# Optimization experiments

Hardware: AMD Instinct MI355X
Metric: run time of the kernel (lower is better)

The kernel has to match this reference:

```python
import jax, jax.numpy as jnp
import numpy as np

S, W = 256, 64          # sentences per doc, words per sentence
V, E = 100000, 256      # vocab, embedding dim
HW, HS, C = 256, 256, 10  # word hidden, sentence hidden, num categories


def _gru_dir(x, Wih, Whh, bih, bhh, reverse):
    """Single-direction GRU, PyTorch gate order (r, z, n). x: [B, T, D] -> [B, T, H]."""
    B, T, D = x.shape
    H = Whh.shape[1]
    xg = jnp.einsum('btd,gd->tbg', x, Wih) + bih  # [T, B, 3H], precompute input gates

    def step(h, xt):
        hg = h @ Whh.T + bhh
        xr, xz, xn = jnp.split(xt, 3, axis=-1)
        hr, hz, hn = jnp.split(hg, 3, axis=-1)
        r = jax.nn.sigmoid(xr + hr)
        z = jax.nn.sigmoid(xz + hz)
        n = jnp.tanh(xn + r * hn)
        h_new = (1.0 - z) * n + z * h
        return h_new, h_new

    h0 = jnp.zeros((B, H), x.dtype)
    _, ys = jax.lax.scan(step, h0, xg, reverse=reverse)  # ys: [T, B, H] in time order
    return jnp.swapaxes(ys, 0, 1)


def _bi_gru(x, WihF, WhhF, bihF, bhhF, WihB, WhhB, bihB, bhhB):
    out_f = _gru_dir(x, WihF, WhhF, bihF, bhhF, reverse=False)
    out_b = _gru_dir(x, WihB, WhhB, bihB, bhhB, reverse=True)
    return jnp.concatenate([out_f, out_b], axis=-1)  # [B, T, 2H]


def _attn_pool(out, w, b):
    # Sequential(Linear(2H,1), Tanh) then softmax over seq dim, weighted sum
    scores = jnp.tanh(out @ w + b)           # [B, T, 1]
    a = jax.nn.softmax(scores, axis=1)       # softmax over time
    return jnp.sum(a * out, axis=1)          # [B, 2H]


def setup_inputs() -> dict:
    key = jax.random.key(0)
    ks = jax.random.split(key, 32)
    sc = 0.05
    d = {
        'tokens': jax.random.randint(ks[0], (S, W), 0, V),
        'emb': jax.random.normal(ks[1], (V, E), jnp.float32) * sc,
        'wWihF': jax.random.normal(ks[2], (3 * HW, E), jnp.float32) * sc,
        'wWhhF': jax.random.normal(ks[3], (3 * HW, HW), jnp.float32) * sc,
        'wBihF': jax.random.normal(ks[4], (3 * HW,), jnp.float32) * sc,
        'wBhhF': jax.random.normal(ks[5], (3 * HW,), jnp.float32) * sc,
        'wWihB': jax.random.normal(ks[6], (3 * HW, E), jnp.float32) * sc,
        'wWhhB': jax.random.normal(ks[7], (3 * HW, HW), jnp.float32) * sc,
        'wBihB': jax.random.normal(ks[8], (3 * HW,), jnp.float32) * sc,
        'wBhhB': jax.random.normal(ks[9], (3 * HW,), jnp.float32) * sc,
        'sWihF': jax.random.normal(ks[10], (3 * HS, 2 * HW), jnp.float32) * sc,
        'sWhhF': jax.random.normal(ks[11], (3 * HS, HS), jnp.float32) * sc,
        'sBihF': jax.random.normal(ks[12], (3 * HS,), jnp.float32) * sc,
        'sBhhF': jax.random.normal(ks[13], (3 * HS,), jnp.float32) * sc,
        'sWihB': jax.random.normal(ks[14], (3 * HS, 2 * HW), jnp.float32) * sc,
        'sWhhB': jax.random.normal(ks[15], (3 * HS, HS), jnp.float32) * sc,
        'sBihB': jax.random.normal(ks[16], (3 * HS,), jnp.float32) * sc,
        'sBhhB': jax.random.normal(ks[17], (3 * HS,), jnp.float32) * sc,
        'wAttW': jax.random.normal(ks[18], (2 * HW, 1), jnp.float32) * sc,
        'wAttB': jax.random.normal(ks[19], (1,), jnp.float32) * sc,
        'sAttW': jax.random.normal(ks[20], (2 * HS, 1), jnp.float32) * sc,
        'sAttB': jax.random.normal(ks[21], (1,), jnp.float32) * sc,
        'clsW': jax.random.normal(ks[22], (C, 2 * HS), jnp.float32) * sc,
        'clsB': jax.random.normal(ks[23], (C,), jnp.float32) * sc,
    }
    return d


def reference(tokens, emb, wWihF, wWhhF, wBihF, wBhhF, wWihB, wWhhB, wBihB, wBhhB,
              sWihF, sWhhF, sBihF, sBhhF, sWihB, sWhhB, sBihB, sBhhB,
              wAttW, wAttB, sAttW, sAttB, clsW, clsB):
    # word level: all sentences batched together (packed form of the Python loop)
    x = emb[tokens]                                             # [S, W, E]
    word_out = _bi_gru(x, wWihF, wWhhF, wBihF, wBhhF, wWihB, wWhhB, wBihB, wBhhB)  # [S, W, 2HW]
    sent_vecs = _attn_pool(word_out, wAttW, wAttB)              # [S, 2HW]
    # sentence level: single document
    sent_in = sent_vecs[None]                                   # [1, S, 2HW]
    sent_out = _bi_gru(sent_in, sWihF, sWhhF, sBihF, sBhhF, sWihB, sWhhB, sBihB, sBhhB)  # [1, S, 2HS]
    doc_vec = _attn_pool(sent_out, sAttW, sAttB)                # [1, 2HS]
    logits = doc_vec @ clsW.T + clsB                            # [1, C]
    return jax.nn.softmax(logits, axis=1)
```

## Files before the change

### kernel.cpp

```cpp
#include <hip/hip_runtime.h>
#include <stdint.h>

typedef unsigned short ushort_t;
typedef uint32_t u32;
typedef __bf16 bf16;
typedef bf16 bf16x8 __attribute__((ext_vector_type(8)));
typedef float f32x4 __attribute__((ext_vector_type(4)));
typedef ushort_t ushort8 __attribute__((ext_vector_type(8)));

__device__ __forceinline__ float b2f(ushort_t u) {
    u32 x = ((u32)u) << 16;
    return __builtin_bit_cast(float, x);
}
__device__ __forceinline__ ushort_t f2b(float f) {
    bf16 h = (bf16)f;
    return __builtin_bit_cast(ushort_t, h);
}
__device__ __forceinline__ float sigmoidf_(float x) { return 1.0f / (1.0f + __expf(-x)); }
__device__ __forceinline__ float tanhf_(float x) { return 1.0f - 2.0f / (1.0f + __expf(2.0f * x)); }

__device__ __forceinline__ ushort8 cvt8(const float* __restrict__ p) {
    float4 v0 = *(const float4*)p;
    float4 v1 = *(const float4*)(p + 4);
    ushort8 r;
    r[0] = f2b(v0.x); r[1] = f2b(v0.y); r[2] = f2b(v0.z); r[3] = f2b(v0.w);
    r[4] = f2b(v1.x); r[5] = f2b(v1.y); r[6] = f2b(v1.z); r[7] = f2b(v1.w);
    return r;
}

#define TPAD 40

__global__ __launch_bounds__(256) void gemm_xg(
    const float* __restrict__ A, const int* __restrict__ tok,
    const float* __restrict__ WF, const float* __restrict__ WB,
    const float* __restrict__ bF, const float* __restrict__ bB,
    ushort_t* __restrict__ C, int K)
{
    __shared__ ushort_t aT[128 * TPAD];
    __shared__ ushort_t bT[128 * TPAD];
    const int tid = threadIdx.x;
    const int lane = tid & 63, wv = tid >> 6;
    const int bn0 = blockIdx.x * 128;
    const int rm0 = blockIdx.y * 128;
    const int wm = (wv & 1) * 64, wn = (wv >> 1) * 64;

    f32x4 acc[4][4];
    f32x4 zero = {0.f, 0.f, 0.f, 0.f};
#pragma unroll
    for (int i = 0; i < 4; i++)
#pragma unroll
        for (int j = 0; j < 4; j++) acc[i][j] = zero;

    const int sr = tid >> 1;
    const int sk = (tid & 1) * 16;
    long arow = tok ? (long)tok[rm0 + sr] : (long)(rm0 + sr);
    const float* aSrc = A + arow * K + sk;
    int ng = bn0 + sr;
    const float* bSrc = (ng < 768 ? WF + (long)ng * K : WB + (long)(ng - 768) * K) + sk;

    const int nkc = K / 32;
    const int fm = lane & 15, fq = (lane >> 4) * 8;
    for (int kc = 0; kc < nkc; ++kc) {
        ushort8 av0 = cvt8(aSrc + kc * 32);
        ushort8 av1 = cvt8(aSrc + kc * 32 + 8);
        ushort8 bv0 = cvt8(bSrc + kc * 32);
        ushort8 bv1 = cvt8(bSrc + kc * 32 + 8);
        __syncthreads();
        *(ushort8*)(aT + sr * TPAD + sk) = av0;
        *(ushort8*)(aT + sr * TPAD + sk + 8) = av1;
        *(ushort8*)(bT + sr * TPAD + sk) = bv0;
        *(ushort8*)(bT + sr * TPAD + sk + 8) = bv1;
        __syncthreads();
        bf16x8 af[4], bfg[4];
#pragma unroll
        for (int i = 0; i < 4; i++)
            af[i] = __builtin_bit_cast(bf16x8, *(const ushort8*)(aT + (wm + i * 16 + fm) * TPAD + fq));
#pragma unroll
        for (int j = 0; j < 4; j++)
            bfg[j] = __builtin_bit_cast(bf16x8, *(const ushort8*)(bT + (wn + j * 16 + fm) * TPAD + fq));
#pragma unroll
        for (int i = 0; i < 4; i++)
#pragma unroll
            for (int j = 0; j < 4; j++)
                acc[i][j] = __builtin_amdgcn_mfma_f32_16x16x32_bf16(af[i], bfg[j], acc[i][j], 0, 0, 0);
    }
    const int fr0 = (lane >> 4) * 4;
#pragma unroll
    for (int j = 0; j < 4; j++) {
        int col = bn0 + wn + j * 16 + fm;
        float bias = (col < 768) ? bF[col] : bB[col - 768];
#pragma unroll
        for (int i = 0; i < 4; i++) {
#pragma unroll
            for (int r = 0; r < 4; r++) {
                int row = rm0 + wm + i * 16 + fr0 + r;
                C[(long)row * 1536 + col] = f2b(acc[i][j][r] + bias);
            }
        }
    }
}

#define HBS 264

template<int NS>
__global__ __launch_bounds__(512, 2) void gru_level(
    const float* __restrict__ WhhF, const float* __restrict__ WhhB,
    const float* __restrict__ bhhF, const float* __restrict__ bhhB,
    const ushort_t* __restrict__ xg,
    ushort_t* __restrict__ out,
    int T)
{
    __shared__ ushort_t hbf[2][16 * HBS];

    const int tid = threadIdx.x, lane = tid & 63, wv = tid >> 6;
    const int dir = blockIdx.x & 1;
    const int grp = blockIdx.x >> 1;
    const float* Whh = dir ? WhhB : WhhF;
    const float* bhh = dir ? bhhB : bhhF;
    const int dirOff = dir * 768;

    const int fm = lane & 15, fq = (lane >> 4) * 8;
    const int mgrp = lane >> 4;
    const int d0 = 32 * wv + fm;

    bf16x8 wfrag[6][8];
#pragma unroll
    for (int g = 0; g < 3; ++g)
#pragma unroll
        for (int t = 0; t < 2; ++t) {
            const float* wrow = Whh + (long)(g * 256 + 32 * wv + 16 * t + fm) * 256 + fq;
#pragma unroll
            for (int kc = 0; kc < 8; ++kc)
                wfrag[g * 2 + t][kc] = __builtin_bit_cast(bf16x8, cvt8(wrow + kc * 32));
        }

    float bhhv[3][2];
#pragma unroll
    for (int g = 0; g < 3; ++g)
#pragma unroll
        for (int t = 0; t < 2; ++t)
            bhhv[g][t] = bhh[g * 256 + d0 + 16 * t];

    for (int i = tid; i < 16 * HBS; i += 512) { hbf[0][i] = 0; hbf[1][i] = 0; }

    const ushort_t* xgm[NS];
    ushort_t* outm[NS];
#pragma unroll
    for (int m = 0; m < NS; ++m) {
        int s = grp * NS + m;
        xgm[m] = xg + (long)s * T * 1536 + dirOff;
        outm[m] = out + (long)s * T * 512 + dir * 256;
    }

    float h[NS][2];
    ushort_t xv[NS][3][2];
    ushort_t ostage[NS][2];
#pragma unroll
    for (int m = 0; m < NS; ++m) { h[m][0] = 0.f; h[m][1] = 0.f; }

    if (mgrp == 0) {
        const int tt0 = dir ? (T - 1) : 0;
#pragma unroll
        for (int m = 0; m < NS; ++m)
#pragma unroll
            for (int g = 0; g < 3; ++g)
#pragma unroll
                for (int t = 0; t < 2; ++t)
                    xv[m][g][t] = xgm[m][(long)tt0 * 1536 + g * 256 + d0 + 16 * t];
    }
    __syncthreads();

    for (int st = 0; st < T; ++st) {
        const int cur = st & 1, nxt = cur ^ 1;
        if (st > 0 && mgrp == 0) {
            const int tp = dir ? (T - st) : (st - 1);
#pragma unroll
            for (int m = 0; m < NS; ++m) {
                outm[m][(long)tp * 512 + d0] = ostage[m][0];
                outm[m][(long)tp * 512 + d0 + 16] = ostage[m][1];
            }
        }
        f32x4 acc[6];
        f32x4 zero = {0.f, 0.f, 0.f, 0.f};
#pragma unroll
        for (int gi = 0; gi < 6; ++gi) acc[gi] = zero;
#pragma unroll
        for (int kc = 0; kc < 8; ++kc) {
            bf16x8 a = __builtin_bit_cast(bf16x8,
                *(const ushort8*)(&hbf[cur][fm * HBS + kc * 32 + fq]));
#pragma unroll
            for (int gi = 0; gi < 6; ++gi)
                acc[gi] = __builtin_amdgcn_mfma_f32_16x16x32_bf16(a, wfrag[gi][kc], acc[gi], 0, 0, 0);
        }
        if (mgrp == 0) {
#pragma unroll
            for (int m = 0; m < NS; ++m)
#pragma unroll
                for (int t = 0; t < 2; ++t) {
                    float xr = b2f(xv[m][0][t]);
                    float xz = b2f(xv[m][1][t]);
                    float xn = b2f(xv[m][2][t]);
                    float r = sigmoidf_(xr + acc[0 + t][m] + bhhv[0][t]);
                    float z = sigmoidf_(xz + acc[2 + t][m] + bhhv[1][t]);
                    float n = tanhf_(xn + r * (acc[4 + t][m] + bhhv[2][t]));
                    h[m][t] = (1.f - z) * n + z * h[m][t];
                    ushort_t hb = f2b(h[m][t]);
                    hbf[nxt][m * HBS + d0 + 16 * t] = hb;
                    ostage[m][t] = hb;
                }
            const int stn = (st + 1 < T) ? (st + 1) : st;
            const int ttn = dir ? (T - 1 - stn) : stn;
#pragma unroll
            for (int m = 0; m < NS; ++m)
#pragma unroll
                for (int g = 0; g < 3; ++g)
#pragma unroll
                    for (int t = 0; t < 2; ++t)
                        xv[m][g][t] = xgm[m][(long)ttn * 1536 + g * 256 + d0 + 16 * t];
        }
        __syncthreads();
    }
    if (mgrp == 0) {
        const int tl = dir ? 0 : (T - 1);
#pragma unroll
        for (int m = 0; m < NS; ++m) {
            outm[m][(long)tl * 512 + d0] = ostage[m][0];
            outm[m][(long)tl * 512 + d0 + 16] = ostage[m][1];
        }
    }
}

__global__ void attn_word(const ushort_t* __restrict__ wout,
                          const float* __restrict__ attW,
                          const float* __restrict__ attB,
                          float* __restrict__ svec)
{
    __shared__ float part[64][4];
    __shared__ float aw[64];
    const int s = blockIdx.x, tid = threadIdx.x;
    const int w = tid >> 2, q = tid & 3;
    const ushort_t* row = wout + ((long)(s * 64 + w)) * 512 + q * 128;
    const float* ap = attW + q * 128;
    float sum = 0.f;
    for (int i = 0; i < 128; i += 8) {
        ushort8 a = *(const ushort8*)(row + i);
        float4 b0 = *(const float4*)(ap + i);
        float4 b1 = *(const float4*)(ap + i + 4);
        sum += b2f(a[0]) * b0.x + b2f(a[1]) * b0.y + b2f(a[2]) * b0.z + b2f(a[3]) * b0.w
             + b2f(a[4]) * b1.x + b2f(a[5]) * b1.y + b2f(a[6]) * b1.z + b2f(a[7]) * b1.w;
    }
    part[w][q] = sum;
    __syncthreads();
    if (tid < 64) {
        float sc = tanhf_(part[tid][0] + part[tid][1] + part[tid][2] + part[tid][3] + attB[0]);
        float m = sc;
#pragma unroll
        for (int o = 32; o >= 1; o >>= 1) m = fmaxf(m, __shfl_xor(m, o, 64));
        float e = __expf(sc - m);
        float se = e;
#pragma unroll
        for (int o = 32; o >= 1; o >>= 1) se += __shfl_xor(se, o, 64);
        aw[tid] = e / se;
    }
    __syncthreads();
    const int d = tid * 2;
    float a0 = 0.f, a1 = 0.f;
    const ushort_t* col = wout + ((long)(s * 64)) * 512 + d;
#pragma unroll 4
    for (int w2 = 0; w2 < 64; ++w2) {
        u32 v = *(const u32*)(col + (long)w2 * 512);
        float wg = aw[w2];
        a0 += wg * b2f((ushort_t)v);
        a1 += wg * b2f((ushort_t)(v >> 16));
    }
    *(float2*)(svec + (long)s * 512 + d) = make_float2(a0, a1);
}

__global__ void attn_sent(const ushort_t* __restrict__ sout,
                          const float* __restrict__ attW,
                          const float* __restrict__ attB,
                          float* __restrict__ doc)
{
    __shared__ float aw[256];
    __shared__ float red[8];
    const int tid = threadIdx.x;
    const ushort_t* row = sout + (long)tid * 512;
    float sum = 0.f;
    for (int i = 0; i < 512; i += 8) {
        ushort8 a = *(const ushort8*)(row + i);
        float4 b0 = *(const float4*)(attW + i);
        float4 b1 = *(const float4*)(attW + i + 4);
        sum += b2f(a[0]) * b0.x + b2f(a[1]) * b0.y + b2f(a[2]) * b0.z + b2f(a[3]) * b0.w
             + b2f(a[4]) * b1.x + b2f(a[5]) * b1.y + b2f(a[6]) * b1.z + b2f(a[7]) * b1.w;
    }
    float sc = tanhf_(sum + attB[0]);
    float m = sc;
#pragma unroll
    for (int o = 32; o >= 1; o >>= 1) m = fmaxf(m, __shfl_xor(m, o, 64));
    if ((tid & 63) == 0) red[tid >> 6] = m;
    __syncthreads();
    m = fmaxf(fmaxf(red[0], red[1]), fmaxf(red[2], red[3]));
    float e = __expf(sc - m);
    float se = e;
#pragma unroll
    for (int o = 32; o >= 1; o >>= 1) se += __shfl_xor(se, o, 64);
    if ((tid & 63) == 0) red[4 + (tid >> 6)] = se;
    __syncthreads();
    se = red[4] + red[5] + red[6] + red[7];
    aw[tid] = e / se;
    __syncthreads();
    const int d = tid * 2;
    float a0 = 0.f, a1 = 0.f;
    for (int t2 = 0; t2 < 256; ++t2) {
        u32 v = *(const u32*)(sout + (long)t2 * 512 + d);
        float w = aw[t2];
        a0 += w * b2f((ushort_t)v);
        a1 += w * b2f((ushort_t)(v >> 16));
    }
    doc[d] = a0;
    doc[d + 1] = a1;
}

__global__ void classify(const float* __restrict__ doc, const float* __restrict__ clsW,
                         const float* __restrict__ clsB, float* __restrict__ outp)
{
    const int lane = threadIdx.x;
    float logit = -1e30f;
    if (lane < 10) {
        float s = clsB[lane];
        const float* wr = clsW + lane * 512;
        for (int i = 0; i < 512; ++i) s += doc[i] * wr[i];
        logit = s;
    }
    float m = logit;
#pragma unroll
    for (int o = 32; o >= 1; o >>= 1) m = fmaxf(m, __shfl_xor(m, o, 64));
    float e = (lane < 10) ? __expf(logit - m) : 0.f;
    float se = e;
#pragma unroll
    for (int o = 32; o >= 1; o >>= 1) se += __shfl_xor(se, o, 64);
    if (lane < 10) outp[lane] = e / se;
}

extern "C" void kernel_launch(void* const* d_in, const int* in_sizes, int n_in,
                              void* d_out, int out_size, void* d_ws, size_t ws_size,
                              hipStream_t stream)
{
    const int*   tokens = (const int*)d_in[0];
    const float* emb    = (const float*)d_in[1];
    const float* wWihF  = (const float*)d_in[2];
    const float* wWhhF  = (const float*)d_in[3];
    const float* wBihF  = (const float*)d_in[4];
    const float* wBhhF  = (const float*)d_in[5];
    const float* wWihB  = (const float*)d_in[6];
    const float* wWhhB  = (const float*)d_in[7];
    const float* wBihB  = (const float*)d_in[8];
    const float* wBhhB  = (const float*)d_in[9];
    const float* sWihF  = (const float*)d_in[10];
    const float* sWhhF  = (const float*)d_in[11];
    const float* sBihF  = (const float*)d_in[12];
    const float* sBhhF  = (const float*)d_in[13];
    const float* sWihB  = (const float*)d_in[14];
    const float* sWhhB  = (const float*)d_in[15];
    const float* sBihB  = (const float*)d_in[16];
    const float* sBhhB  = (const float*)d_in[17];
    const float* wAttW  = (const float*)d_in[18];
    const float* wAttB  = (const float*)d_in[19];
    const float* sAttW  = (const float*)d_in[20];
    const float* sAttB  = (const float*)d_in[21];
    const float* clsW   = (const float*)d_in[22];
    const float* clsB   = (const float*)d_in[23];

    char* ws = (char*)d_ws;
    ushort_t* xg   = (ushort_t*)(ws);
    ushort_t* wout = (ushort_t*)(ws + 50331648);
    float*    svec = (float*)(ws + 67108864);
    ushort_t* sxg  = (ushort_t*)(ws + 67633152);
    ushort_t* sout = (ushort_t*)(ws + 68419584);
    float*    doc  = (float*)(ws + 68681728);

    gemm_xg<<<dim3(12, 128), 256, 0, stream>>>(emb, tokens, wWihF, wWihB, wBihF, wBihB, xg, 256);
    gru_level<2><<<256, 512, 0, stream>>>(wWhhF, wWhhB, wBhhF, wBhhB, xg, wout, 64);
    attn_word<<<256, 256, 0, stream>>>(wout, wAttW, wAttB, svec);
    gemm_xg<<<dim3(12, 2), 256, 0, stream>>>(svec, nullptr, sWihF, sWihB, sBihF, sBihB, sxg, 512);
    gru_level<1><<<2, 512, 0, stream>>>(sWhhF, sWhhB, sBhhF, sBhhB, sxg, sout, 256);
    attn_sent<<<1, 256, 0, stream>>>(sout, sAttW, sAttB, doc);
    classify<<<1, 64, 0, stream>>>(doc, clsW, clsB, (float*)d_out);
}
```

Measured before the change: 951.0 us.

## Stage GRU input gates and outputs through shared-memory chunks with double buffering

The recurrent GRU kernel now loads the precomputed input-gate activations for a chunk of CS timesteps cooperatively into shared memory, using all 512 threads and 16-byte vector loads. The next chunk is prefetched while the current one is processed. Hidden outputs are buffered in shared memory and written back per chunk as coalesced vector stores. This replaces the per-step scalar global loads and stores issued by only one quarter of the lanes. It removes global latency from the serial per-step critical path at the cost of more shared memory per block, which may reduce occupancy under the two-blocks-per-CU launch bound.

After: 842.5 us. -11.4%, faster.

```diff
diff --git a/kernel.cpp b/kernel.cpp
--- a/kernel.cpp
+++ b/kernel.cpp
@@ -101,8 +101,10 @@
 }
 
 #define HBS 264
-
-template<int NS>
+#define XRS 776
+#define ORS 264
+
+template<int NS, int CS>
 __global__ __launch_bounds__(512, 2) void gru_level(
     const float* __restrict__ WhhF, const float* __restrict__ WhhB,
     const float* __restrict__ bhhF, const float* __restrict__ bhhB,
@@ -111,6 +113,8 @@
     int T)
 {
     __shared__ ushort_t hbf[2][16 * HBS];
+    __shared__ ushort_t xch[2][16 * XRS];
+    __shared__ ushort_t och[2][16 * ORS];
 
     const int tid = threadIdx.x, lane = tid & 63, wv = tid >> 6;
     const int dir = blockIdx.x & 1;
@@ -143,91 +147,92 @@
 
     for (int i = tid; i < 16 * HBS; i += 512) { hbf[0][i] = 0; hbf[1][i] = 0; }
 
-    const ushort_t* xgm[NS];
-    ushort_t* outm[NS];
-#pragma unroll
-    for (int m = 0; m < NS; ++m) {
-        int s = grp * NS + m;
-        xgm[m] = xg + (long)s * T * 1536 + dirOff;
-        outm[m] = out + (long)s * T * 512 + dir * 256;
-    }
+    const int s0 = grp * NS;
+    const ushort_t* xgm0 = xg + (long)s0 * T * 1536 + dirOff;
+    const ushort_t* xgm1 = xg + (long)(s0 + (NS > 1 ? 1 : 0)) * T * 1536 + dirOff;
+    ushort_t* outm0 = out + (long)s0 * T * 512 + dir * 256;
+    ushort_t* outm1 = out + (long)(s0 + (NS > 1 ? 1 : 0)) * T * 512 + dir * 256;
 
     float h[NS][2];
-    ushort_t xv[NS][3][2];
-    ushort_t ostage[NS][2];
 #pragma unroll
     for (int m = 0; m < NS; ++m) { h[m][0] = 0.f; h[m][1] = 0.f; }
 
-    if (mgrp == 0) {
-        const int tt0 = dir ? (T - 1) : 0;
-#pragma unroll
-        for (int m = 0; m < NS; ++m)
-#pragma unroll
-            for (int g = 0; g < 3; ++g)
-#pragma unroll
-                for (int t = 0; t < 2; ++t)
-                    xv[m][g][t] = xgm[m][(long)tt0 * 1536 + g * 256 + d0 + 16 * t];
-    }
-    __syncthreads();
-
-    for (int st = 0; st < T; ++st) {
-        const int cur = st & 1, nxt = cur ^ 1;
-        if (st > 0 && mgrp == 0) {
-            const int tp = dir ? (T - st) : (st - 1);
-#pragma unroll
-            for (int m = 0; m < NS; ++m) {
-                outm[m][(long)tp * 512 + d0] = ostage[m][0];
-                outm[m][(long)tp * 512 + d0 + 16] = ostage[m][1];
+    const int nch = T / CS;
+
+    auto stage_x = [&](int c2) {
+        ushort8 val[3];
+        int row[3], c8[3];
+#pragma unroll
+        for (int i = 0; i < 3; ++i) {
+            int v = tid + i * 512;
+            row[i] = v / 96; c8[i] = v - row[i] * 96;
+            int sc = row[i] / NS, m = row[i] - sc * NS;
+            int stg = c2 * CS + sc;
+            int tt = dir ? (T - 1 - stg) : stg;
+            const ushort_t* xp = (NS == 1 || m == 0) ? xgm0 : xgm1;
+            val[i] = *(const ushort8*)(xp + (long)tt * 1536 + c8[i] * 8);
+        }
+#pragma unroll
+        for (int i = 0; i < 3; ++i)
+            *(ushort8*)(&xch[c2 & 1][row[i] * XRS + c8[i] * 8]) = val[i];
+    };
+
+    auto flush_o = [&](int c2) {
+        int v = tid;
+        int row = v >> 5, c8 = v & 31;
+        int sc = row / NS, m = row - sc * NS;
+        int stg = c2 * CS + sc;
+        int tt = dir ? (T - 1 - stg) : stg;
+        ushort8 val = *(const ushort8*)(&och[c2 & 1][row * ORS + c8 * 8]);
+        ushort_t* op = (NS == 1 || m == 0) ? outm0 : outm1;
+        *(ushort8*)(op + (long)tt * 512 + c8 * 8) = val;
+    };
+
+    stage_x(0);
+    __syncthreads();
+
+    for (int c = 0; c < nch; ++c) {
+        const int buf = c & 1;
+        if (c > 0) flush_o(c - 1);
+        if (c + 1 < nch) stage_x(c + 1);
+        for (int sc = 0; sc < CS; ++sc) {
+            const int st = c * CS + sc;
+            const int cur = st & 1, nxt = cur ^ 1;
+            f32x4 acc[6];
+            f32x4 zero = {0.f, 0.f, 0.f, 0.f};
+#pragma unroll
+            for (int gi = 0; gi < 6; ++gi) acc[gi] = zero;
+#pragma unroll
+            for (int kc = 0; kc < 8; ++kc) {
+                bf16x8 a = __builtin_bit_cast(bf16x8,
+                    *(const ushort8*)(&hbf[cur][fm * HBS + kc * 32 + fq]));
+#pragma unroll
+                for (int gi = 0; gi < 6; ++gi)
+                    acc[gi] = __builtin_amdgcn_mfma_f32_16x16x32_bf16(a, wfrag[gi][kc], acc[gi], 0, 0, 0);
             }
+            if (mgrp == 0) {
+#pragma unroll
+                for (int m = 0; m < NS; ++m) {
+                    const int xrow = (sc * NS + m) * XRS;
+#pragma unroll
+                    for (int t = 0; t < 2; ++t) {
+                        float xr = b2f(xch[buf][xrow + d0 + 16 * t]);
+                        float xz = b2f(xch[buf][xrow + 256 + d0 + 16 * t]);
+                        float xn = b2f(xch[buf][xrow + 512 + d0 + 16 * t]);
+                        float r = sigmoidf_(xr + acc[0 + t][m] + bhhv[0][t]);
+                        float z = sigmoidf_(xz + acc[2 + t][m] + bhhv[1][t]);
+                        float n = tanhf_(xn + r * (acc[4 + t][m] + bhhv[2][t]));
+                        h[m][t] = (1.f - z) * n + z * h[m][t];
+                        ushort_t hb = f2b(h[m][t]);
+                        hbf[nxt][m * HBS + d0 + 16 * t] = hb;
+                        och[buf][(sc * NS + m) * ORS + d0 + 16 * t] = hb;
+                    }
+                }
+            }
+            __syncthreads();
         }
-        f32x4 acc[6];
-        f32x4 zero = {0.f, 0.f, 0.f, 0.f};
-#pragma unroll
-        for (int gi = 0; gi < 6; ++gi) acc[gi] = zero;
-#pragma unroll
-        for (int kc = 0; kc < 8; ++kc) {
-            bf16x8 a = __builtin_bit_cast(bf16x8,
-                *(const ushort8*)(&hbf[cur][fm * HBS + kc * 32 + fq]));
-#pragma unroll
-            for (int gi = 0; gi < 6; ++gi)
-                acc[gi] = __builtin_amdgcn_mfma_f32_16x16x32_bf16(a, wfrag[gi][kc], acc[gi], 0, 0, 0);
-        }
-        if (mgrp == 0) {
-#pragma unroll
-            for (int m = 0; m < NS; ++m)
-#pragma unroll
-                for (int t = 0; t < 2; ++t) {
-                    float xr = b2f(xv[m][0][t]);
-                    float xz = b2f(xv[m][1][t]);
-                    float xn = b2f(xv[m][2][t]);
-                    float r = sigmoidf_(xr + acc[0 + t][m] + bhhv[0][t]);
-                    float z = sigmoidf_(xz + acc[2 + t][m] + bhhv[1][t]);
-                    float n = tanhf_(xn + r * (acc[4 + t][m] + bhhv[2][t]));
-                    h[m][t] = (1.f - z) * n + z * h[m][t];
-                    ushort_t hb = f2b(h[m][t]);
-                    hbf[nxt][m * HBS + d0 + 16 * t] = hb;
-                    ostage[m][t] = hb;
-                }
-            const int stn = (st + 1 < T) ? (st + 1) : st;
-            const int ttn = dir ? (T - 1 - stn) : stn;
-#pragma unroll
-            for (int m = 0; m < NS; ++m)
-#pragma unroll
-                for (int g = 0; g < 3; ++g)
-#pragma unroll
-                    for (int t = 0; t < 2; ++t)
-                        xv[m][g][t] = xgm[m][(long)ttn * 1536 + g * 256 + d0 + 16 * t];
-        }
-        __syncthreads();
-    }
-    if (mgrp == 0) {
-        const int tl = dir ? 0 : (T - 1);
-#pragma unroll
-        for (int m = 0; m < NS; ++m) {
-            outm[m][(long)tl * 512 + d0] = ostage[m][0];
-            outm[m][(long)tl * 512 + d0 + 16] = ostage[m][1];
-        }
-    }
+    }
+    flush_o(nch - 1);
 }
 
 __global__ void attn_word(const ushort_t* __restrict__ wout,
@@ -380,10 +385,10 @@
     float*    doc  = (float*)(ws + 68681728);
 
     gemm_xg<<<dim3(12, 128), 256, 0, stream>>>(emb, tokens, wWihF, wWihB, wBihF, wBihB, xg, 256);
-    gru_level<2><<<256, 512, 0, stream>>>(wWhhF, wWhhB, wBhhF, wBhhB, xg, wout, 64);
+    gru_level<2, 8><<<256, 512, 0, stream>>>(wWhhF, wWhhB, wBhhF, wBhhB, xg, wout, 64);
     attn_word<<<256, 256, 0, stream>>>(wout, wAttW, wAttB, svec);
     gemm_xg<<<dim3(12, 2), 256, 0, stream>>>(svec, nullptr, sWihF, sWihB, sBihF, sBihB, sxg, 512);
-    gru_level<1><<<2, 512, 0, stream>>>(sWhhF, sWhhB, sBhhF, sBhhB, sxg, sout, 256);
+    gru_level<1, 16><<<2, 512, 0, stream>>>(sWhhF, sWhhB, sBhhF, sBhhB, sxg, sout, 256);
     attn_sent<<<1, 256, 0, stream>>>(sout, sAttW, sAttB, doc);
     classify<<<1, 64, 0, stream>>>(doc, clsW, clsB, (float*)d_out);
 }
```
